# Kernel tuning notes

Hardware: AMD Instinct MI355X
Metric: run time of the kernel (lower is better)

Reference implementation:

```python
import jax, jax.numpy as jnp
import numpy as np

# w_mul = gain * 5**-0.5 * lrmul with gain=sqrt(2), use_wscale=True, lrmul=1
W_MUL = float(2 ** 0.5 * 5 ** -0.5)


def _apply_1q(M, g, q):
    """Apply 2x2 gate g on qubit q (MSB-first) to the rows of matrix M (dim, dim)."""
    dim = M.shape[0]
    Mr = M.reshape(2 ** q, 2, -1)  # (pre, 2, post*dim)
    return jnp.einsum('ab,xby->xay', g, Mr).reshape(dim, dim)


def _fused_xyz_gates(th, n):
    """Per-qubit fused gate Rz(tz) @ Ry(ty) @ Rx(tx); th = [tx_0..n, ty_0..n, tz_0..n]."""
    hx, hy, hz = th[:n] / 2, th[n:2 * n] / 2, th[2 * n:] / 2
    cx, sx = jnp.cos(hx), jnp.sin(hx)
    cy, sy = jnp.cos(hy), jnp.sin(hy)
    z = jnp.zeros_like(hz)
    gx = jnp.stack([jnp.stack([cx + 0j, -1j * sx], -1),
                    jnp.stack([-1j * sx, cx + 0j], -1)], -2)
    gy = jnp.stack([jnp.stack([cy + 0j, -sy + 0j], -1),
                    jnp.stack([sy + 0j, cy + 0j], -1)], -2)
    ez = jnp.exp(-1j * hz)
    gz = jnp.stack([jnp.stack([ez, z + 0j], -1),
                    jnp.stack([z + 0j, jnp.conj(ez)], -1)], -2)
    return jnp.einsum('nab,nbc,ncd->nad', gz, gy, gx).astype(jnp.complex64)


def _cnot_perm(n, c, t):
    """Row permutation implementing CNOT(control=c, target=t), MSB-first bit order."""
    r = np.arange(2 ** n)
    return r ^ (((r >> (n - 1 - c)) & 1) << (n - 1 - t))


def _build_U(weight):
    n = weight.shape[0] // 15
    dim = 2 ** n
    w = weight * W_MUL
    ring_perms = [jnp.asarray(_cnot_perm(n, c, (c + 1) % n)) for c in range(n)]
    U = jnp.eye(dim, dtype=jnp.complex64)
    for layer in range(5):  # 5 XYZ layers, rings of CNOT between them
        g = _fused_xyz_gates(w[3 * n * layer:3 * n * (layer + 1)], n)
        for q in range(n):
            U = _apply_1q(U, g[q], q)
        if layer < 4:
            for p in ring_perms:
                U = U[p]  # CNOT is a row permutation
    return U


def setup_inputs() -> dict:
    key = jax.random.key(0)
    k1, k2 = jax.random.split(key)
    n_qubits = 11
    dim = 2 ** n_qubits
    x = jax.random.normal(k1, (dim, dim), dtype=jnp.float32)
    weight = jax.random.uniform(k2, (15 * n_qubits,), dtype=jnp.float32,
                                minval=0.0, maxval=2.0 * np.pi)
    return {"x": x, "weight": weight}


def reference(x, weight):
    U = _build_U(weight)
    xc = x.astype(jnp.complex64)
    return U @ xc @ U.conj().T
```

## Files before the change

kernel.cpp:

```cpp
#include <hip/hip_runtime.h>

typedef unsigned short u16;
typedef __attribute__((ext_vector_type(8))) short bf16x8;
typedef __attribute__((ext_vector_type(4))) float f32x4;
typedef __attribute__((ext_vector_type(4))) unsigned int u32x4;

#define DIM 2048

__device__ inline u16 f2bf(float f) {
    unsigned u = __builtin_bit_cast(unsigned, f);
    u = (u + 0x7FFFu + ((u >> 16) & 1u)) >> 16;
    return (u16)u;
}

__device__ inline void gl_lds16(const void* g, void* l) {
    __builtin_amdgcn_global_load_lds(
        (const __attribute__((address_space(1))) unsigned int*)g,
        (__attribute__((address_space(3))) unsigned int*)l, 16, 0, 0);
}

struct c32 { float x, y; };
__device__ inline c32 cmul(c32 a, c32 b) { return {a.x*b.x - a.y*b.y, a.x*b.y + a.y*b.x}; }

__device__ inline int slot2(int i) { return i + (i >> 4); }

__device__ inline void bfly(float2 g0, float2 g1, float2 g2, float2 g3,
                            float2& u, float2& w) {
    float2 nu, nw;
    nu.x = g0.x*u.x - g0.y*u.y + g1.x*w.x - g1.y*w.y;
    nu.y = g0.x*u.y + g0.y*u.x + g1.x*w.y + g1.y*w.x;
    nw.x = g2.x*u.x - g2.y*u.y + g3.x*w.x - g3.y*w.y;
    nw.y = g2.x*u.y + g2.y*u.x + g3.x*w.y + g3.y*w.x;
    u = nu; w = nw;
}

__global__ __launch_bounds__(256) void build_ut(const float* __restrict__ w,
                                                u16* __restrict__ ut_re,
                                                u16* __restrict__ ut_im) {
    __shared__ alignas(16) float2 gg[55][4];
    __shared__ alignas(16) u16 ptab[DIM];
    __shared__ alignas(16) float2 V[DIM + (DIM >> 4)];
    const int tid = threadIdx.x;
    const int col = blockIdx.x;

    if (tid < 55) {
        const int layer = tid / 11, q = tid - layer * 11;
        const float WM = 0.63245553203367586f;
        float hx = 0.5f * WM * w[33*layer + q];
        float hy = 0.5f * WM * w[33*layer + 11 + q];
        float hz = 0.5f * WM * w[33*layer + 22 + q];
        float cx = cosf(hx), sx = sinf(hx);
        float cy = cosf(hy), sy = sinf(hy);
        float cz = cosf(hz), sz = sinf(hz);
        c32 m00{cy*cx,  sy*sx}, m01{-sy*cx, -cy*sx};
        c32 m10{sy*cx, -cy*sx}, m11{ cy*cx, -sy*sx};
        c32 em{cz, -sz}, ep{cz, sz};
        c32 r0 = cmul(em, m00), r1 = cmul(em, m01);
        c32 r2 = cmul(ep, m10), r3 = cmul(ep, m11);
        gg[tid][0] = make_float2(r0.x, r0.y);
        gg[tid][1] = make_float2(r1.x, r1.y);
        gg[tid][2] = make_float2(r2.x, r2.y);
        gg[tid][3] = make_float2(r3.x, r3.y);
    }
    for (int i = tid; i < DIM; i += 256) {
        V[slot2(i)] = make_float2((i == col) ? 1.0f : 0.0f, 0.0f);
        int jj = i;
        #pragma unroll
        for (int c = 10; c >= 0; --c) {
            int sc = 10 - c;
            int st = 10 - ((c + 1) % 11);
            jj ^= ((jj >> sc) & 1) << st;
        }
        ptab[i] = (u16)slot2(jj);
    }
    __syncthreads();

    auto round3 = [&](int b2, int b1, int b0, int gq2, int gq1, int gq0,
                      bool permRead) {
        int x = tid;
        x = ((x >> b0) << (b0 + 1)) | (x & ((1 << b0) - 1));
        x = ((x >> b1) << (b1 + 1)) | (x & ((1 << b1) - 1));
        x = ((x >> b2) << (b2 + 1)) | (x & ((1 << b2) - 1));
        float2 v[8]; int sl[8];
        #pragma unroll
        for (int j = 0; j < 8; ++j) {
            int e = x | ((j >> 2) << b2) | (((j >> 1) & 1) << b1) | ((j & 1) << b0);
            sl[j] = slot2(e);
            v[j] = V[permRead ? (int)ptab[e] : sl[j]];
        }
        if (permRead) __syncthreads();
        {   float2 g0 = gg[gq2][0], g1 = gg[gq2][1], g2 = gg[gq2][2], g3 = gg[gq2][3];
            bfly(g0,g1,g2,g3, v[0], v[4]); bfly(g0,g1,g2,g3, v[1], v[5]);
            bfly(g0,g1,g2,g3, v[2], v[6]); bfly(g0,g1,g2,g3, v[3], v[7]); }
        {   float2 g0 = gg[gq1][0], g1 = gg[gq1][1], g2 = gg[gq1][2], g3 = gg[gq1][3];
            bfly(g0,g1,g2,g3, v[0], v[2]); bfly(g0,g1,g2,g3, v[1], v[3]);
            bfly(g0,g1,g2,g3, v[4], v[6]); bfly(g0,g1,g2,g3, v[5], v[7]); }
        {   float2 g0 = gg[gq0][0], g1 = gg[gq0][1], g2 = gg[gq0][2], g3 = gg[gq0][3];
            bfly(g0,g1,g2,g3, v[0], v[1]); bfly(g0,g1,g2,g3, v[2], v[3]);
            bfly(g0,g1,g2,g3, v[4], v[5]); bfly(g0,g1,g2,g3, v[6], v[7]); }
        #pragma unroll
        for (int j = 0; j < 8; ++j) V[sl[j]] = v[j];
        __syncthreads();
    };

    auto round2 = [&](int gq1, int gq0) {
        float2 g10 = gg[gq1][0], g11 = gg[gq1][1], g12 = gg[gq1][2], g13 = gg[gq1][3];
        float2 g00 = gg[gq0][0], g01 = gg[gq0][1], g02 = gg[gq0][2], g03 = gg[gq0][3];
        #pragma unroll
        for (int h = 0; h < 2; ++h) {
            int i0 = (tid + h * 256) << 2;
            float2 v[4]; int sl[4];
            #pragma unroll
            for (int j = 0; j < 4; ++j) { sl[j] = slot2(i0 | j); v[j] = V[sl[j]]; }
            bfly(g10,g11,g12,g13, v[0], v[2]); bfly(g10,g11,g12,g13, v[1], v[3]);
            bfly(g00,g01,g02,g03, v[0], v[1]); bfly(g00,g01,g02,g03, v[2], v[3]);
            #pragma unroll
            for (int j = 0; j < 4; ++j) V[sl[j]] = v[j];
        }
        __syncthreads();
    };

    for (int layer = 0; layer < 5; ++layer) {
        const int gb = layer * 11;
        round3(10, 9, 8, gb + 0, gb + 1, gb + 2, layer > 0);
        round3( 7, 6, 5, gb + 3, gb + 4, gb + 5, false);
        round3( 4, 3, 2, gb + 6, gb + 7, gb + 8, false);
        round2(gb + 9, gb + 10);
    }
    for (int i = tid; i < DIM; i += 256) {
        float2 v = V[slot2(i)];
        ut_re[(size_t)col*DIM + i] = f2bf(v.x);
        ut_im[(size_t)col*DIM + i] = f2bf(v.y);
    }
}

__global__ __launch_bounds__(256) void transpose2(const u16* __restrict__ sre,
                                                  const u16* __restrict__ sim,
                                                  u16* __restrict__ dre,
                                                  u16* __restrict__ dim_) {
    const u16* s = blockIdx.z ? sim : sre;
    u16*       d = blockIdx.z ? dim_ : dre;
    __shared__ alignas(16) u16 tile[64][66];
    const int bx = blockIdx.x * 64, by = blockIdx.y * 64;
    for (int e = threadIdx.x; e < 1024; e += 256) {
        int r = e >> 4, c4 = (e & 15) * 4;
        uint2 v = *(const uint2*)(s + (size_t)(by + r) * DIM + bx + c4);
        u16* tp = &tile[r][c4];
        tp[0] = (u16)(v.x); tp[1] = (u16)(v.x >> 16);
        tp[2] = (u16)(v.y); tp[3] = (u16)(v.y >> 16);
    }
    __syncthreads();
    for (int e = threadIdx.x; e < 1024; e += 256) {
        int r = e >> 4, c4 = (e & 15) * 4;
        unsigned lo = (unsigned)tile[c4][r]     | ((unsigned)tile[c4+1][r] << 16);
        unsigned hi = (unsigned)tile[c4+2][r]   | ((unsigned)tile[c4+3][r] << 16);
        *(uint2*)(d + (size_t)(bx + r) * DIM + by + c4) = make_uint2(lo, hi);
    }
}

__global__ __launch_bounds__(256, 2) void gemm_stage1(
        const u16* __restrict__ ure, const u16* __restrict__ uim,
        const float* __restrict__ x,
        u16* __restrict__ pt, u16* __restrict__ qt) {
    __shared__ alignas(16) u16 Ab[2][2][128*32], Bx[2][2][128*32];
    const u16* A  = blockIdx.z ? uim : ure;
    u16*      dst = blockIdx.z ? qt  : pt;
    const int tid  = threadIdx.x;
    const int lane = tid & 63, w = tid >> 6;
    const int m0 = blockIdx.y * 128, n0 = blockIdx.x * 128;
    const int wm = (w >> 1) * 64, wn = (w & 1) * 64;
    const int ml = lane & 15, quad = lane >> 4;

    f32x4 acc[4][4];
    #pragma unroll
    for (int i = 0; i < 4; ++i)
        #pragma unroll
        for (int j = 0; j < 4; ++j) {
            f32x4 z = {0.f, 0.f, 0.f, 0.f};
            acc[i][j] = z;
        }

    auto stage = [&](int b, int k0) {
        #pragma unroll
        for (int pn = 0; pn < 2; ++pn) {
            #pragma unroll
            for (int t = 0; t < 2; ++t) {
                int ci = t * 256 + tid;
                int r = ci >> 2, c = ci & 3;
                size_t goA = ((size_t)(m0 + r) * DIM + k0 + pn * 32) * 2 + c * 16;
                gl_lds16((const char*)A + goA, (char*)Ab[b][pn] + ci * 16);
                const float4* src = (const float4*)(x + (size_t)(n0 + r) * DIM + k0 + pn * 32 + c * 8);
                float4 v0 = src[0], v1 = src[1];
                u32x4 pk;
                pk.x = (unsigned)f2bf(v0.x) | ((unsigned)f2bf(v0.y) << 16);
                pk.y = (unsigned)f2bf(v0.z) | ((unsigned)f2bf(v0.w) << 16);
                pk.z = (unsigned)f2bf(v1.x) | ((unsigned)f2bf(v1.y) << 16);
                pk.w = (unsigned)f2bf(v1.z) | ((unsigned)f2bf(v1.w) << 16);
                *(u32x4*)((char*)Bx[b][pn] + ci * 16) = pk;
            }
        }
    };

    stage(0, 0);
    __syncthreads();

    for (int k0 = 0; k0 < DIM; k0 += 64) {
        const int cb = (k0 >> 6) & 1;
        if (k0 + 64 < DIM) stage(cb ^ 1, k0 + 64);

        #pragma unroll
        for (int pn = 0; pn < 2; ++pn) {
            bf16x8 af[4], bf[4];
            #pragma unroll
            for (int i = 0; i < 4; ++i) {
                af[i] = *(const bf16x8*)(Ab[cb][pn] + (wm + i*16 + ml) * 32 + quad * 8);
                bf[i] = *(const bf16x8*)(Bx[cb][pn] + (wn + i*16 + ml) * 32 + quad * 8);
            }
            #pragma unroll
            for (int i = 0; i < 4; ++i)
                #pragma unroll
                for (int j = 0; j < 4; ++j)
                    acc[i][j] = __builtin_amdgcn_mfma_f32_16x16x32_bf16(af[i], bf[j], acc[i][j], 0, 0, 0);
        }
        __syncthreads();
    }
    #pragma unroll
    for (int i = 0; i < 4; ++i)
        #pragma unroll
        for (int j = 0; j < 4; ++j) {
            int row = m0 + wm + i*16 + quad*4;
            int col = n0 + wn + j*16 + ml;
            #pragma unroll
            for (int r = 0; r < 4; ++r)
                dst[(size_t)(row + r) * DIM + col] = f2bf(acc[i][j][r]);
        }
}

__global__ __launch_bounds__(256, 2) void gemm_stage2_atomic(
        const u16* __restrict__ ure, const u16* __restrict__ uim,
        const u16* __restrict__ pt, const u16* __restrict__ qt,
        float* __restrict__ out) {
    __shared__ alignas(16) u16 Ab[2][2][128*32], Bb[2][2][128*32];
    const u16* A = blockIdx.z ? uim : ure;
    const u16* B = blockIdx.z ? qt  : pt;
    const int tid  = threadIdx.x;
    const int lane = tid & 63, w = tid >> 6;
    const int m0 = blockIdx.y * 128, n0 = blockIdx.x * 128;
    const int wm = (w >> 1) * 64, wn = (w & 1) * 64;
    const int ml = lane & 15, quad = lane >> 4;

    f32x4 acc[4][4];
    #pragma unroll
    for (int i = 0; i < 4; ++i)
        #pragma unroll
        for (int j = 0; j < 4; ++j) {
            f32x4 z = {0.f, 0.f, 0.f, 0.f};
            acc[i][j] = z;
        }

    auto stage = [&](int b, int k0) {
        #pragma unroll
        for (int pn = 0; pn < 2; ++pn) {
            #pragma unroll
            for (int t = 0; t < 2; ++t) {
                int ci = t * 256 + tid;
                int r = ci >> 2, c = ci & 3;
                size_t goA = ((size_t)(m0 + r) * DIM + k0 + pn * 32) * 2 + c * 16;
                size_t goB = ((size_t)(n0 + r) * DIM + k0 + pn * 32) * 2 + c * 16;
                gl_lds16((const char*)A + goA, (char*)Ab[b][pn] + ci * 16);
                gl_lds16((const char*)B + goB, (char*)Bb[b][pn] + ci * 16);
            }
        }
    };

    stage(0, 0);
    __syncthreads();

    for (int k0 = 0; k0 < DIM; k0 += 64) {
        const int cb = (k0 >> 6) & 1;
        if (k0 + 64 < DIM) stage(cb ^ 1, k0 + 64);

        #pragma unroll
        for (int pn = 0; pn < 2; ++pn) {
            bf16x8 af[4], bf[4];
            #pragma unroll
            for (int i = 0; i < 4; ++i) {
                af[i] = *(const bf16x8*)(Ab[cb][pn] + (wm + i*16 + ml) * 32 + quad * 8);
                bf[i] = *(const bf16x8*)(Bb[cb][pn] + (wn + i*16 + ml) * 32 + quad * 8);
            }
            #pragma unroll
            for (int i = 0; i < 4; ++i)
                #pragma unroll
                for (int j = 0; j < 4; ++j)
                    acc[i][j] = __builtin_amdgcn_mfma_f32_16x16x32_bf16(af[i], bf[j], acc[i][j], 0, 0, 0);
        }
        __syncthreads();
    }
    #pragma unroll
    for (int i = 0; i < 4; ++i)
        #pragma unroll
        for (int j = 0; j < 4; ++j) {
            int row = m0 + wm + i*16 + quad*4;
            int col = n0 + wn + j*16 + ml;
            #pragma unroll
            for (int r = 0; r < 4; ++r)
                unsafeAtomicAdd(&out[(size_t)(row + r) * DIM + col], acc[i][j][r]);
        }
}

__global__ __launch_bounds__(256, 1) void gemm_stage2_cplx(
        const u16* __restrict__ ure, const u16* __restrict__ uim,
        const u16* __restrict__ pt, const u16* __restrict__ qt,
        float2* __restrict__ out, size_t out_lim) {
    __shared__ alignas(16) u16 Ar[128*32], Ai[128*32], Bp[128*32], Bq[128*32];
    const int tid  = threadIdx.x;
    const int lane = tid & 63, w = tid >> 6;
    const int m0 = blockIdx.y * 128, n0 = blockIdx.x * 128;
    const int wm = (w >> 1) * 64, wn = (w & 1) * 64;
    const int ml = lane & 15, quad = lane >> 4;

    f32x4 accR[4][4], accI[4][4];
    #pragma unroll
    for (int i = 0; i < 4; ++i)
        #pragma unroll
        for (int j = 0; j < 4; ++j) {
            f32x4 z = {0.f, 0.f, 0.f, 0.f};
            accR[i][j] = z; accI[i][j] = z;
        }

    for (int k0 = 0; k0 < DIM; k0 += 32) {
        #pragma unroll
        for (int t = 0; t < 2; ++t) {
            int ci = t * 256 + tid;
            int r = ci >> 2, c = ci & 3;
            size_t goA = ((size_t)(m0 + r) * DIM + k0) * 2 + c * 16;
            size_t goB = ((size_t)(n0 + r) * DIM + k0) * 2 + c * 16;
            gl_lds16((const char*)ure + goA, (char*)Ar + ci * 16);
            gl_lds16((const char*)uim + goA, (char*)Ai + ci * 16);
            gl_lds16((const char*)pt  + goB, (char*)Bp + ci * 16);
            gl_lds16((const char*)qt  + goB, (char*)Bq + ci * 16);
        }
        __syncthreads();
        bf16x8 ar[4], ai[4], bp[4], bq[4];
        #pragma unroll
        for (int i = 0; i < 4; ++i) {
            ar[i] = *(const bf16x8*)(Ar + (wm + i*16 + ml) * 32 + quad * 8);
            ai[i] = *(const bf16x8*)(Ai + (wm + i*16 + ml) * 32 + quad * 8);
            bp[i] = *(const bf16x8*)(Bp + (wn + i*16 + ml) * 32 + quad * 8);
            bq[i] = *(const bf16x8*)(Bq + (wn + i*16 + ml) * 32 + quad * 8);
        }
        #pragma unroll
        for (int i = 0; i < 4; ++i)
            #pragma unroll
            for (int j = 0; j < 4; ++j) {
                accR[i][j] = __builtin_amdgcn_mfma_f32_16x16x32_bf16(ar[i], bp[j], accR[i][j], 0, 0, 0);
                accR[i][j] = __builtin_amdgcn_mfma_f32_16x16x32_bf16(ai[i], bq[j], accR[i][j], 0, 0, 0);
                accI[i][j] = __builtin_amdgcn_mfma_f32_16x16x32_bf16(ai[i], bp[j], accI[i][j], 0, 0, 0);
                f32x4 t2 = __builtin_amdgcn_mfma_f32_16x16x32_bf16(ar[i], bq[j], {0.f,0.f,0.f,0.f}, 0, 0, 0);
                accI[i][j] -= t2;
            }
        __syncthreads();
    }
    #pragma unroll
    for (int i = 0; i < 4; ++i)
        #pragma unroll
        for (int j = 0; j < 4; ++j) {
            int row = m0 + wm + i*16 + quad*4;
            int col = n0 + wn + j*16 + ml;
            #pragma unroll
            for (int r = 0; r < 4; ++r) {
                size_t idx = (size_t)(row + r) * DIM + col;
                if (idx < out_lim)
                    out[idx] = make_float2(accR[i][j][r], accI[i][j][r]);
            }
        }
}

extern "C" void kernel_launch(void* const* d_in, const int* in_sizes, int n_in,
                              void* d_out, int out_size, void* d_ws, size_t ws_size,
                              hipStream_t stream) {
    int xi = (in_sizes[0] >= in_sizes[1]) ? 0 : 1;
    const float* x = (const float*)d_in[xi];
    const float* w = (const float*)d_in[1 - xi];

    char* ws = (char*)d_ws;
    const size_t P = (size_t)DIM * DIM * 2;
    if (ws_size < 4 * P) return;

    u16* ut_re = (u16*)(ws);
    u16* ut_im = (u16*)(ws + P);
    u16* u_re  = (u16*)(ws + 2*P);
    u16* u_im  = (u16*)(ws + 3*P);
    u16* pt    = ut_re;
    u16* qt    = ut_im;

    build_ut<<<DIM, 256, 0, stream>>>(w, ut_re, ut_im);
    transpose2<<<dim3(32, 32, 2), 256, 0, stream>>>(ut_re, ut_im, u_re, u_im);
    gemm_stage1<<<dim3(16, 16, 2), 256, 0, stream>>>(u_re, u_im, x, pt, qt);

    if (out_size == DIM * DIM) {
        hipMemsetAsync(d_out, 0, (size_t)DIM * DIM * sizeof(float), stream);
        gemm_stage2_atomic<<<dim3(16, 16, 2), 256, 0, stream>>>(u_re, u_im, pt, qt,
                                                                (float*)d_out);
    } else {
        gemm_stage2_cplx<<<dim3(16, 16), 256, 0, stream>>>(u_re, u_im, pt, qt,
                                                           (float2*)d_out,
                                                           (size_t)out_size / 2);
    }
}
```

Measured before the change: 264.3 us.

## Analytically initialize first gate layer, simplify CNOT ring permutation, pre-convert x to bf16

Starting from a basis column, the first XYZ layer's output is a tensor product of gate columns, so it is now written directly as products of gate entries instead of running the butterfly rounds for layer 0. The CNOT ring permutation table is replaced by a closed-form bit expression. The fp32-to-bf16 conversion of x moves out of gemm_stage1 into a separate x2bf kernel, so the GEMM can load both operands with direct global-to-LDS loads and stops repeating the conversion for every tile that reuses x. The trade-offs are an extra launch, an extra pass over x, and a fallback that borrows d_out as scratch space when the workspace is too small.

```diff
diff --git a/kernel.cpp b/kernel.cpp
--- a/kernel.cpp
+++ b/kernel.cpp
@@ -21,6 +21,9 @@
 
 struct c32 { float x, y; };
 __device__ inline c32 cmul(c32 a, c32 b) { return {a.x*b.x - a.y*b.y, a.x*b.y + a.y*b.x}; }
+__device__ inline float2 cmulf2(float2 a, float2 b) {
+    return make_float2(a.x*b.x - a.y*b.y, a.x*b.y + a.y*b.x);
+}
 
 __device__ inline int slot2(int i) { return i + (i >> 4); }
 
@@ -63,15 +66,35 @@
         gg[tid][3] = make_float2(r3.x, r3.y);
     }
     for (int i = tid; i < DIM; i += 256) {
-        V[slot2(i)] = make_float2((i == col) ? 1.0f : 0.0f, 0.0f);
-        int jj = i;
-        #pragma unroll
-        for (int c = 10; c >= 0; --c) {
-            int sc = 10 - c;
-            int st = 10 - ((c + 1) % 11);
-            jj ^= ((jj >> sc) & 1) << st;
-        }
+        int jj = (i ^ (i >> 1)) ^ ((i & 1) ? 0x600 : 0);
         ptab[i] = (u16)slot2(jj);
+    }
+    __syncthreads();
+
+    {
+        float2 p = gg[0][((((tid >> 7) & 1) << 1)) | ((col >> 10) & 1)];
+        #pragma unroll
+        for (int b = 9; b >= 3; --b) {
+            float2 ge = gg[10 - b][(((tid >> (b - 3)) & 1) << 1) | ((col >> b) & 1)];
+            p = cmulf2(p, ge);
+        }
+        const int c2 = (col >> 2) & 1, c1 = (col >> 1) & 1, c0 = col & 1;
+        float2 a0  = cmulf2(p, gg[8][c2]);
+        float2 a1  = cmulf2(p, gg[8][2 | c2]);
+        float2 b00 = cmulf2(a0, gg[9][c1]);
+        float2 b01 = cmulf2(a0, gg[9][2 | c1]);
+        float2 b10 = cmulf2(a1, gg[9][c1]);
+        float2 b11 = cmulf2(a1, gg[9][2 | c1]);
+        float2 g0 = gg[10][c0], g1 = gg[10][2 | c0];
+        const int base = tid << 3;
+        V[slot2(base + 0)] = cmulf2(b00, g0);
+        V[slot2(base + 1)] = cmulf2(b00, g1);
+        V[slot2(base + 2)] = cmulf2(b01, g0);
+        V[slot2(base + 3)] = cmulf2(b01, g1);
+        V[slot2(base + 4)] = cmulf2(b10, g0);
+        V[slot2(base + 5)] = cmulf2(b10, g1);
+        V[slot2(base + 6)] = cmulf2(b11, g0);
+        V[slot2(base + 7)] = cmulf2(b11, g1);
     }
     __syncthreads();
 
@@ -120,9 +143,9 @@
         __syncthreads();
     };
 
-    for (int layer = 0; layer < 5; ++layer) {
+    for (int layer = 1; layer < 5; ++layer) {
         const int gb = layer * 11;
-        round3(10, 9, 8, gb + 0, gb + 1, gb + 2, layer > 0);
+        round3(10, 9, 8, gb + 0, gb + 1, gb + 2, true);
         round3( 7, 6, 5, gb + 3, gb + 4, gb + 5, false);
         round3( 4, 3, 2, gb + 6, gb + 7, gb + 8, false);
         round2(gb + 9, gb + 10);
@@ -158,9 +181,22 @@
     }
 }
 
+__global__ __launch_bounds__(256) void x2bf(const float* __restrict__ x,
+                                            u16* __restrict__ xb) {
+    const int i = (blockIdx.x * 256 + threadIdx.x) * 8;
+    const float4* s = (const float4*)(x + i);
+    float4 v0 = s[0], v1 = s[1];
+    u32x4 pk;
+    pk.x = (unsigned)f2bf(v0.x) | ((unsigned)f2bf(v0.y) << 16);
+    pk.y = (unsigned)f2bf(v0.z) | ((unsigned)f2bf(v0.w) << 16);
+    pk.z = (unsigned)f2bf(v1.x) | ((unsigned)f2bf(v1.y) << 16);
+    pk.w = (unsigned)f2bf(v1.z) | ((unsigned)f2bf(v1.w) << 16);
+    *(u32x4*)(xb + i) = pk;
+}
+
 __global__ __launch_bounds__(256, 2) void gemm_stage1(
         const u16* __restrict__ ure, const u16* __restrict__ uim,
-        const float* __restrict__ x,
+        const u16* __restrict__ xb,
         u16* __restrict__ pt, u16* __restrict__ qt) {
     __shared__ alignas(16) u16 Ab[2][2][128*32], Bx[2][2][128*32];
     const u16* A  = blockIdx.z ? uim : ure;
@@ -188,15 +224,9 @@
                 int ci = t * 256 + tid;
                 int r = ci >> 2, c = ci & 3;
                 size_t goA = ((size_t)(m0 + r) * DIM + k0 + pn * 32) * 2 + c * 16;
-                gl_lds16((const char*)A + goA, (char*)Ab[b][pn] + ci * 16);
-                const float4* src = (const float4*)(x + (size_t)(n0 + r) * DIM + k0 + pn * 32 + c * 8);
-                float4 v0 = src[0], v1 = src[1];
-                u32x4 pk;
-                pk.x = (unsigned)f2bf(v0.x) | ((unsigned)f2bf(v0.y) << 16);
-                pk.y = (unsigned)f2bf(v0.z) | ((unsigned)f2bf(v0.w) << 16);
-                pk.z = (unsigned)f2bf(v1.x) | ((unsigned)f2bf(v1.y) << 16);
-                pk.w = (unsigned)f2bf(v1.z) | ((unsigned)f2bf(v1.w) << 16);
-                *(u32x4*)((char*)Bx[b][pn] + ci * 16) = pk;
+                size_t goB = ((size_t)(n0 + r) * DIM + k0 + pn * 32) * 2 + c * 16;
+                gl_lds16((const char*)A  + goA, (char*)Ab[b][pn] + ci * 16);
+                gl_lds16((const char*)xb + goB, (char*)Bx[b][pn] + ci * 16);
             }
         }
     };
@@ -393,10 +423,12 @@
     u16* u_im  = (u16*)(ws + 3*P);
     u16* pt    = ut_re;
     u16* qt    = ut_im;
+    u16* xb = (ws_size >= 5 * P) ? (u16*)(ws + 4*P) : (u16*)d_out;
 
     build_ut<<<DIM, 256, 0, stream>>>(w, ut_re, ut_im);
     transpose2<<<dim3(32, 32, 2), 256, 0, stream>>>(ut_re, ut_im, u_re, u_im);
-    gemm_stage1<<<dim3(16, 16, 2), 256, 0, stream>>>(u_re, u_im, x, pt, qt);
+    x2bf<<<DIM*DIM/(256*8), 256, 0, stream>>>(x, xb);
+    gemm_stage1<<<dim3(16, 16, 2), 256, 0, stream>>>(u_re, u_im, xb, pt, qt);
 
     if (out_size == DIM * DIM) {
         hipMemsetAsync(d_out, 0, (size_t)DIM * DIM * sizeof(float), stream);
```

Measured after the change: 246.0 us. -6.9%, faster.
